# Kernel tuning notes

Measured on AMD Instinct MI355X. Metric: run time of the kernel, lower is better.

Reference implementation:

```python
import jax, jax.numpy as jnp
import numpy as np

B_SZ, L, H, D, N, R, K = 2, 1024, 2048, 4096, 16, 128, 4


def setup_inputs() -> dict:
    key = jax.random.key(0)
    ks = jax.random.split(key, 10)
    s = lambda *sh: 1.0 / np.sqrt(sh[-1])
    inp = {
        "hidden_states": jax.random.normal(ks[0], (B_SZ, L, H), jnp.float32),
        "in_proj_w": jax.random.normal(ks[1], (2 * D, H), jnp.float32) * s(H),
        "conv_w": jax.random.normal(ks[2], (D, 1, K), jnp.float32) * s(K),
        "conv_b": jax.random.normal(ks[3], (D,), jnp.float32) * 0.02,
        "x_proj_w": jax.random.normal(ks[4], (R + 2 * N, D), jnp.float32) * s(D),
        "dt_proj_w": jax.random.normal(ks[5], (D, R), jnp.float32) * s(R),
        "dt_proj_b": jax.random.normal(ks[6], (D,), jnp.float32) * 0.02,
        # A_log = log(arange(1, N+1)) broadcast over D, as in the module init
        "A_log": jnp.broadcast_to(jnp.log(jnp.arange(1, N + 1, dtype=jnp.float32))[None, :], (D, N)),
        "D_param": jnp.ones((D,), jnp.float32),
        "out_proj_w": jax.random.normal(ks[7], (H, D), jnp.float32) * s(D),
    }
    return inp


def _mamba_forward(hidden_states, in_proj_w, conv_w, conv_b, x_proj_w,
                   dt_proj_w, dt_proj_b, A_log, D_param, out_proj_w):
    silu = jax.nn.silu
    # in_proj: [B,L,H] @ [H,2D] -> [B,L,2D] -> [B,2D,L]
    proj = jnp.einsum("blh,ph->bpl", hidden_states, in_proj_w)
    u, gate = jnp.split(proj, 2, axis=1)  # each [B,D,L]
    # depthwise causal conv1d (padding K-1 on the left, then first L outputs)
    u = jax.lax.conv_general_dilated(
        u, conv_w, window_strides=(1,), padding=[(K - 1, 0)],
        dimension_numbers=("NCH", "OIH", "NCH"), feature_group_count=D,
    ) + conv_b[None, :, None]
    u = silu(u)  # [B,D,L]
    # x_proj on [B,L,D]
    ssm_params = jnp.einsum("bdl,pd->blp", u, x_proj_w)  # [B,L,R+2N]
    time_step, Bmat, Cmat = jnp.split(ssm_params, [R, R + N], axis=-1)
    # dt_proj + softplus -> [B,D,L]
    dt = jnp.einsum("blr,dr->bld", time_step, dt_proj_w) + dt_proj_b
    dt = jax.nn.softplus(dt).transpose(0, 2, 1)  # [B,D,L]
    A = -jnp.exp(A_log)  # [D,N]

    # selective scan over time; carry ssm_state [B,D,N]
    def step(state, xs):
        dt_t, B_t, C_t, u_t = xs  # [B,D],[B,N],[B,N],[B,D]
        dA = jnp.exp(A[None] * dt_t[:, :, None])          # [B,D,N]
        dBu = dt_t[:, :, None] * B_t[:, None, :] * u_t[:, :, None]
        state = dA * state + dBu
        y_t = jnp.einsum("bdn,bn->bd", state, C_t)        # [B,D]
        return state, y_t

    xs = (dt.transpose(2, 0, 1),          # [L,B,D]
          Bmat.transpose(1, 0, 2),        # [L,B,N]
          Cmat.transpose(1, 0, 2),        # [L,B,N]
          u.transpose(2, 0, 1))           # [L,B,D]
    init = jnp.zeros((hidden_states.shape[0], D, N), hidden_states.dtype)
    _, ys = jax.lax.scan(step, init, xs)   # ys [L,B,D]
    y = ys.transpose(1, 2, 0)              # [B,D,L]
    y = y + u * D_param[None, :, None]
    y = y * silu(gate)
    # out_proj: [B,L,D] @ [D,H]
    return jnp.einsum("bdl,hd->blh", y, out_proj_w)


def reference(hidden_states, in_proj_w, conv_w, conv_b, x_proj_w,
              dt_proj_w, dt_proj_b, A_log, D_param, out_proj_w):
    return _mamba_forward(hidden_states, in_proj_w, conv_w, conv_b, x_proj_w,
                          dt_proj_w, dt_proj_b, A_log, D_param, out_proj_w)
```

## Files before the change

### kernel.cpp

```cpp
#include <hip/hip_runtime.h>

#define L_SEQ 1024
#define DD 4096
#define NC 32
#define CT 32

typedef short bf16x8 __attribute__((ext_vector_type(8)));
typedef float f32x4 __attribute__((ext_vector_type(4)));
typedef unsigned short u16;

typedef const __attribute__((address_space(1))) void gas_t;
typedef __attribute__((address_space(3))) void las_t;

__device__ inline u16 f2bf(float f) {
  unsigned int u = __float_as_uint(f);
  u = (u + 0x7FFFu + ((u >> 16) & 1u)) >> 16;
  return (u16)u;
}

__device__ inline float bf2f(u16 v) {
  return __uint_as_float(((unsigned int)v) << 16);
}

__device__ inline float softplusf(float x) {
  return x > 20.f ? x : log1pf(expf(x));
}

__global__ __launch_bounds__(256) void cast_bf16_k(const float* __restrict__ s,
                                                   u16* __restrict__ d, int n) {
  int i = (blockIdx.x * 256 + threadIdx.x) * 4;
  if (i >= n) return;
  float4 v = *(const float4*)(s + i);
  ushort4 o;
  o.x = f2bf(v.x); o.y = f2bf(v.y); o.z = f2bf(v.z); o.w = f2bf(v.w);
  *(ushort4*)(d + i) = o;
}

__global__ __launch_bounds__(256) void reduce4_k(const float* __restrict__ p,
                                                 float* __restrict__ out,
                                                 long n) {
  long i = ((long)blockIdx.x * 256 + threadIdx.x) * 4;
  if (i >= n) return;
  float4 a = *(const float4*)(p + i);
  float4 b = *(const float4*)(p + n + i);
  float4 c = *(const float4*)(p + 2 * n + i);
  float4 d = *(const float4*)(p + 3 * n + i);
  float4 o;
  o.x = (a.x + b.x) + (c.x + d.x);
  o.y = (a.y + b.y) + (c.y + d.y);
  o.z = (a.z + b.z) + (c.z + d.z);
  o.w = (a.w + b.w) + (c.w + d.w);
  *(float4*)(out + i) = o;
}

template <int CMODE, bool SWZ>
__global__ __launch_bounds__(512, 2) void gemm256(const u16* __restrict__ A,
                                                  const u16* __restrict__ B,
                                                  void* __restrict__ Cv,
                                                  int Nld, int K, int kc,
                                                  long zstride) {
  __shared__ u16 lds[2][2][8192];
  const int tid = threadIdx.x;
  const int lane = tid & 63, wid = tid >> 6;
  const int wm = wid >> 2, wn = wid & 3;
  int ty = blockIdx.y, tx = blockIdx.x;
  if (SWZ) {
    int flat = blockIdx.y * 32 + blockIdx.x;
    int xcd = flat & 7, pos = flat >> 3;
    ty = (xcd & 1) * 4 + (pos >> 3);
    tx = (xcd >> 1) * 8 + (pos & 7);
  }
  const long tm = (long)ty * 256, tn = (long)tx * 256;

  const int ksw = ((lane >> 4) ^ (lane & 3) ^ ((lane >> 2) & 3)) * 8;

  const long ks0 = (CMODE == 2) ? (long)blockIdx.z * kc : 0;

  const int srow = tid >> 2;
  const u16* gA0 = A + (tm + srow) * (long)K + ks0 + ksw;
  const u16* gA1 = A + (tm + 128 + srow) * (long)K + ks0 + ksw;
  const u16* gB0 = B + (tn + srow) * (long)K + ks0 + ksw;
  const u16* gB1 = B + (tn + 128 + srow) * (long)K + ks0 + ksw;
  const int sb0 = wid * 512;
  const int sb1 = 4096 + wid * 512;

  f32x4 acc[8][4] = {};

  const int lr = lane & 15;
  const int arow = wm * 128 + lr;
  const int brow = wn * 64 + lr;

  const int KT = kc >> 5;
  int cur = 0;
  __builtin_amdgcn_global_load_lds((gas_t*)gA0, (las_t*)&lds[0][0][sb0], 16, 0, 0);
  __builtin_amdgcn_global_load_lds((gas_t*)gA1, (las_t*)&lds[0][0][sb1], 16, 0, 0);
  __builtin_amdgcn_global_load_lds((gas_t*)gB0, (las_t*)&lds[0][1][sb0], 16, 0, 0);
  __builtin_amdgcn_global_load_lds((gas_t*)gB1, (las_t*)&lds[0][1][sb1], 16, 0, 0);
  __syncthreads();

  for (int kt = 0; kt < KT; ++kt) {
    if (kt + 1 < KT) {
      const long ko = (long)(kt + 1) << 5;
      const int nb = cur ^ 1;
      __builtin_amdgcn_global_load_lds((gas_t*)(gA0 + ko), (las_t*)&lds[nb][0][sb0], 16, 0, 0);
      __builtin_amdgcn_global_load_lds((gas_t*)(gA1 + ko), (las_t*)&lds[nb][0][sb1], 16, 0, 0);
      __builtin_amdgcn_global_load_lds((gas_t*)(gB0 + ko), (las_t*)&lds[nb][1][sb0], 16, 0, 0);
      __builtin_amdgcn_global_load_lds((gas_t*)(gB1 + ko), (las_t*)&lds[nb][1][sb1], 16, 0, 0);
    }
    bf16x8 af[8], bfr[4];
#pragma unroll
    for (int n = 0; n < 4; n++)
      bfr[n] = *(const bf16x8*)&lds[cur][1][(brow + n * 16) * 32 + ksw];
#pragma unroll
    for (int m = 0; m < 8; m++)
      af[m] = *(const bf16x8*)&lds[cur][0][(arow + m * 16) * 32 + ksw];
#pragma unroll
    for (int m = 0; m < 8; m++)
#pragma unroll
      for (int n = 0; n < 4; n++)
        acc[m][n] = __builtin_amdgcn_mfma_f32_16x16x32_bf16(af[m], bfr[n],
                                                            acc[m][n], 0, 0, 0);
    __syncthreads();
    cur ^= 1;
  }

  float* Cf = (CMODE == 2) ? (float*)Cv + (long)blockIdx.z * zstride
                           : (float*)Cv;

  const int rg = (lane >> 4) * 4;
#pragma unroll
  for (int m = 0; m < 8; m++) {
    const long gr = tm + wm * 128 + m * 16 + rg;
#pragma unroll
    for (int n = 0; n < 4; n++) {
      const long gc = tn + wn * 64 + n * 16 + lr;
#pragma unroll
      for (int r = 0; r < 4; r++) {
        if (CMODE == 1)
          ((u16*)Cv)[(gr + r) * (long)Nld + gc] = f2bf(acc[m][n][r]);
        else
          Cf[(gr + r) * (long)Nld + gc] = acc[m][n][r];
      }
    }
  }
}

template <bool CLAMP_N, bool SPLITK, bool SOFTPLUS, bool OUTBF>
__global__ __launch_bounds__(256) void gemm_bt(const u16* __restrict__ A,
                                               const u16* __restrict__ B,
                                               void* __restrict__ Cv,
                                               const float* __restrict__ ebias,
                                               int Nv, int K, int ldc, int kc) {
  __shared__ u16 lA[128 * 32];
  __shared__ u16 lB[128 * 32];
  const int tid = threadIdx.x;
  const int lane = tid & 63, wid = tid >> 6;
  const int wm = wid >> 1, wn = wid & 1;
  const long tm = (long)blockIdx.y * 128, tn = (long)blockIdx.x * 128;

  f32x4 acc[4][4] = {};

  const int rowoff = lane >> 2;
  const int ko = (lane & 3) * 8;
  const int c0 = wid * 2, c1 = c0 + 1;
  const long ra0 = tm + c0 * 16 + rowoff;
  const long ra1 = tm + c1 * 16 + rowoff;
  long rb0 = tn + c0 * 16 + rowoff;
  long rb1 = tn + c1 * 16 + rowoff;
  if (CLAMP_N) {
    if (rb0 >= Nv) rb0 = Nv - 1;
    if (rb1 >= Nv) rb1 = Nv - 1;
  }
  const u16* gA0 = A + ra0 * K + ko;
  const u16* gA1 = A + ra1 * K + ko;
  const u16* gB0 = B + rb0 * K + ko;
  const u16* gB1 = B + rb1 * K + ko;
  u16* sA0 = &lA[c0 * 512];
  u16* sA1 = &lA[c1 * 512];
  u16* sB0 = &lB[c0 * 512];
  u16* sB1 = &lB[c1 * 512];

  int ks0 = 0, ks1 = K;
  if (SPLITK) { ks0 = blockIdx.z * kc; ks1 = ks0 + kc; }

  const int lr = lane & 15, kq = (lane >> 4) * 8;
  const int arow = wm * 64 + lr, brow = wn * 64 + lr;

  for (int ks = ks0; ks < ks1; ks += 32) {
    __builtin_amdgcn_global_load_lds((gas_t*)(gA0 + ks), (las_t*)sA0, 16, 0, 0);
    __builtin_amdgcn_global_load_lds((gas_t*)(gA1 + ks), (las_t*)sA1, 16, 0, 0);
    __builtin_amdgcn_global_load_lds((gas_t*)(gB0 + ks), (las_t*)sB0, 16, 0, 0);
    __builtin_amdgcn_global_load_lds((gas_t*)(gB1 + ks), (las_t*)sB1, 16, 0, 0);
    __syncthreads();
    bf16x8 af[4], bfr[4];
#pragma unroll
    for (int i = 0; i < 4; i++) {
      af[i]  = *(const bf16x8*)&lA[(arow + i * 16) * 32 + kq];
      bfr[i] = *(const bf16x8*)&lB[(brow + i * 16) * 32 + kq];
    }
#pragma unroll
    for (int i = 0; i < 4; i++)
#pragma unroll
      for (int j = 0; j < 4; j++)
        acc[i][j] = __builtin_amdgcn_mfma_f32_16x16x32_bf16(af[i], bfr[j],
                                                            acc[i][j], 0, 0, 0);
    __syncthreads();
  }

  const int rg = (lane >> 4) * 4;
#pragma unroll
  for (int i = 0; i < 4; i++) {
    const long gr = tm + wm * 64 + i * 16 + rg;
#pragma unroll
    for (int j = 0; j < 4; j++) {
      const long gc = tn + wn * 64 + j * 16 + lr;
      if (CLAMP_N && gc >= Nv) continue;
      float bias = 0.f;
      if (SOFTPLUS) bias = ebias[gc];
#pragma unroll
      for (int r = 0; r < 4; r++) {
        float v = acc[i][j][r];
        if (SOFTPLUS) v = softplusf(v + bias);
        if (SPLITK) atomicAdd((float*)Cv + (gr + r) * (long)ldc + gc, v);
        else if (OUTBF) ((u16*)Cv)[(gr + r) * (long)ldc + gc] = f2bf(v);
        else ((float*)Cv)[(gr + r) * (long)ldc + gc] = v;
      }
    }
  }
}

__global__ __launch_bounds__(256) void conv_silu_k(const u16* __restrict__ projb,
                                                   const float* __restrict__ cw,
                                                   const float* __restrict__ cb,
                                                   u16* __restrict__ ub) {
  const int idx = blockIdx.x * 256 + threadIdx.x;
  const int d = idx & (DD - 1);
  const int bl = idx >> 12;
  const int l = bl & (L_SEQ - 1);
  const float4 w = *(const float4*)(cw + d * 4);
  float s = cb[d];
  const u16* pp = projb + (long)bl * 8192 + d;
  s += w.w * bf2f(pp[0]);
  if (l >= 1) s += w.z * bf2f(pp[-8192]);
  if (l >= 2) s += w.y * bf2f(pp[-2 * 8192]);
  if (l >= 3) s += w.x * bf2f(pp[-3 * 8192]);
  const float r = s / (1.f + expf(-s));
  ub[idx] = f2bf(r);
}

__global__ __launch_bounds__(256) void ts_extract_k(const float* __restrict__ ssm,
                                                    u16* __restrict__ ts) {
  int idx = blockIdx.x * 256 + threadIdx.x;
  int row = idx >> 7, r = idx & 127;
  ts[idx] = f2bf(ssm[row * 160 + r]);
}

__global__ __launch_bounds__(256) void scan_p1(const u16* __restrict__ dt,
                                               const u16* __restrict__ u,
                                               const float* __restrict__ ssm,
                                               const float* __restrict__ A_log,
                                               float* __restrict__ Sbuf,
                                               float* __restrict__ Pbuf) {
  __shared__ float sBC[CT * 32];
  const int tid = threadIdx.x;
  const int d = blockIdx.x * 256 + tid;
  const int c = blockIdx.y, b = blockIdx.z;
  const long blbase = (long)b * L_SEQ + (long)c * CT;
  for (int i = tid; i < CT * 32; i += 256) {
    int tt = i >> 5, j = i & 31;
    sBC[i] = ssm[(blbase + tt) * 160 + 128 + j];
  }
  __syncthreads();
  float a2[16], st[16], pr[16];
#pragma unroll
  for (int g = 0; g < 4; g++) {
    float4 al = *(const float4*)(A_log + d * 16 + g * 4);
    a2[g*4+0] = -expf(al.x) * 1.4426950408889634f;
    a2[g*4+1] = -expf(al.y) * 1.4426950408889634f;
    a2[g*4+2] = -expf(al.z) * 1.4426950408889634f;
    a2[g*4+3] = -expf(al.w) * 1.4426950408889634f;
  }
#pragma unroll
  for (int n = 0; n < 16; n++) { st[n] = 0.f; pr[n] = 1.f; }
  for (int tt = 0; tt < CT; tt++) {
    const long bl = blbase + tt;
    const float dtv = bf2f(dt[bl * DD + d]);
    const float uv = bf2f(u[bl * DD + d]);
    const float dtu = dtv * uv;
    const float4* Bv = (const float4*)&sBC[tt * 32];
#pragma unroll
    for (int g = 0; g < 4; g++) {
      const float4 Bg = Bv[g];
      float e;
      e = exp2f(a2[g*4+0]*dtv); st[g*4+0] = e*st[g*4+0] + dtu*Bg.x; pr[g*4+0] *= e;
      e = exp2f(a2[g*4+1]*dtv); st[g*4+1] = e*st[g*4+1] + dtu*Bg.y; pr[g*4+1] *= e;
      e = exp2f(a2[g*4+2]*dtv); st[g*4+2] = e*st[g*4+2] + dtu*Bg.z; pr[g*4+2] *= e;
      e = exp2f(a2[g*4+3]*dtv); st[g*4+3] = e*st[g*4+3] + dtu*Bg.w; pr[g*4+3] *= e;
    }
  }
  const long base = (((long)b * NC + c) * DD + d) * 16;
#pragma unroll
  for (int g = 0; g < 4; g++) {
    *(float4*)(Sbuf + base + g * 4) = make_float4(st[g*4+0], st[g*4+1], st[g*4+2], st[g*4+3]);
    *(float4*)(Pbuf + base + g * 4) = make_float4(pr[g*4+0], pr[g*4+1], pr[g*4+2], pr[g*4+3]);
  }
}

__global__ __launch_bounds__(256) void scan_p2(const float* __restrict__ Sbuf,
                                               const float* __restrict__ Pbuf,
                                               float* __restrict__ carry) {
  const int idx = blockIdx.x * 256 + threadIdx.x;
  const int ng = idx & 3;
  const int d = (idx >> 2) & (DD - 1);
  const int b = idx >> 14;
  float4 cr = make_float4(0.f, 0.f, 0.f, 0.f);
  for (int c = 0; c < NC; c++) {
    const long base = (((long)b * NC + c) * DD + d) * 16 + ng * 4;
    *(float4*)(carry + base) = cr;
    const float4 P = *(const float4*)(Pbuf + base);
    const float4 S = *(const float4*)(Sbuf + base);
    cr.x = P.x * cr.x + S.x;
    cr.y = P.y * cr.y + S.y;
    cr.z = P.z * cr.z + S.z;
    cr.w = P.w * cr.w + S.w;
  }
}

__global__ __launch_bounds__(256) void scan_p3(const u16* __restrict__ dt,
                                               const u16* __restrict__ u,
                                               const float* __restrict__ ssm,
                                               const u16* __restrict__ projb,
                                               const float* __restrict__ A_log,
                                               const float* __restrict__ Dp,
                                               const float* __restrict__ carry,
                                               u16* __restrict__ yb) {
  __shared__ float sBC[CT * 32];
  const int tid = threadIdx.x;
  const int d = blockIdx.x * 256 + tid;
  const int c = blockIdx.y, b = blockIdx.z;
  const long blbase = (long)b * L_SEQ + (long)c * CT;
  for (int i = tid; i < CT * 32; i += 256) {
    int tt = i >> 5, j = i & 31;
    sBC[i] = ssm[(blbase + tt) * 160 + 128 + j];
  }
  __syncthreads();
  float a2[16], st[16];
#pragma unroll
  for (int g = 0; g < 4; g++) {
    float4 al = *(const float4*)(A_log + d * 16 + g * 4);
    a2[g*4+0] = -expf(al.x) * 1.4426950408889634f;
    a2[g*4+1] = -expf(al.y) * 1.4426950408889634f;
    a2[g*4+2] = -expf(al.z) * 1.4426950408889634f;
    a2[g*4+3] = -expf(al.w) * 1.4426950408889634f;
  }
  const long cbase = (((long)b * NC + c) * DD + d) * 16;
#pragma unroll
  for (int g = 0; g < 4; g++) {
    float4 cv = *(const float4*)(carry + cbase + g * 4);
    st[g*4+0] = cv.x; st[g*4+1] = cv.y; st[g*4+2] = cv.z; st[g*4+3] = cv.w;
  }
  const float dp = Dp[d];
  for (int tt = 0; tt < CT; tt++) {
    const long bl = blbase + tt;
    const float dtv = bf2f(dt[bl * DD + d]);
    const float uv = bf2f(u[bl * DD + d]);
    const float dtu = dtv * uv;
    float acc = 0.f;
    const float4* Bv = (const float4*)&sBC[tt * 32];
    const float4* Cv = Bv + 4;
#pragma unroll
    for (int g = 0; g < 4; g++) {
      const float4 Bg = Bv[g];
      const float4 Cg = Cv[g];
      float e;
      e = exp2f(a2[g*4+0]*dtv); st[g*4+0] = e*st[g*4+0] + dtu*Bg.x; acc += st[g*4+0]*Cg.x;
      e = exp2f(a2[g*4+1]*dtv); st[g*4+1] = e*st[g*4+1] + dtu*Bg.y; acc += st[g*4+1]*Cg.y;
      e = exp2f(a2[g*4+2]*dtv); st[g*4+2] = e*st[g*4+2] + dtu*Bg.z; acc += st[g*4+2]*Cg.z;
      e = exp2f(a2[g*4+3]*dtv); st[g*4+3] = e*st[g*4+3] + dtu*Bg.w; acc += st[g*4+3]*Cg.w;
    }
    const float g = bf2f(projb[bl * 8192 + DD + d]);
    const float yv = (acc + uv * dp) * (g / (1.f + expf(-g)));
    yb[bl * DD + d] = f2bf(yv);
  }
}

extern "C" void kernel_launch(void* const* d_in, const int* in_sizes, int n_in,
                              void* d_out, int out_size, void* d_ws, size_t ws_size,
                              hipStream_t stream) {
  const float* hs     = (const float*)d_in[0];
  const float* w_in   = (const float*)d_in[1];
  const float* conv_w = (const float*)d_in[2];
  const float* conv_b = (const float*)d_in[3];
  const float* xw     = (const float*)d_in[4];
  const float* dtw    = (const float*)d_in[5];
  const float* dtb    = (const float*)d_in[6];
  const float* A_log  = (const float*)d_in[7];
  const float* Dp     = (const float*)d_in[8];
  const float* ow     = (const float*)d_in[9];
  float* out = (float*)d_out;

  constexpr size_t SZ_HS_BF  = 2048ull * 2048 * 2;
  constexpr size_t SZ_WIN_BF = 8192ull * 2048 * 2;
  constexpr size_t SZ_PROJ   = 2048ull * 8192 * 2;
  constexpr size_t SZ_UBF    = 2048ull * 4096 * 2;
  constexpr size_t SZ_XW_BF  = 160ull * 4096 * 2;
  constexpr size_t SZ_SSM    = 2048ull * 160 * 4;
  constexpr size_t SZ_TS_BF  = 2048ull * 128 * 2;
  constexpr size_t SZ_DTW_BF = 4096ull * 128 * 2;
  constexpr size_t SZ_DT     = 2048ull * 4096 * 2;
  constexpr size_t SZ_OW_BF  = 2048ull * 4096 * 2;
  constexpr size_t SZ_YBF    = 2048ull * 4096 * 2;
  constexpr size_t SZ_SCAN   = 2ull * NC * DD * 16 * 4;
  constexpr size_t TOTAL = SZ_HS_BF + SZ_WIN_BF + SZ_PROJ + SZ_UBF +
                           SZ_XW_BF + SZ_SSM + SZ_TS_BF + SZ_DTW_BF + SZ_DT +
                           SZ_OW_BF + SZ_YBF + 3 * SZ_SCAN;
  if (ws_size < TOTAL) return;

  char* w = (char*)d_ws;
  u16* hs_bf   = (u16*)w;   w += SZ_HS_BF;
  u16* win_bf  = (u16*)w;   w += SZ_WIN_BF;
  u16* projb   = (u16*)w;   w += SZ_PROJ;
  u16* u_bf    = (u16*)w;   w += SZ_UBF;
  u16* xw_bf   = (u16*)w;   w += SZ_XW_BF;
  float* ssm   = (float*)w; w += SZ_SSM;
  u16* ts_bf   = (u16*)w;   w += SZ_TS_BF;
  u16* dtw_bf  = (u16*)w;   w += SZ_DTW_BF;
  u16* dt_bf   = (u16*)w;   w += SZ_DT;
  u16* ow_bf   = (u16*)w;   w += SZ_OW_BF;
  u16* y_bf    = (u16*)w;   w += SZ_YBF;
  float* Sbuf  = (float*)w; w += SZ_SCAN;
  float* Pbuf  = (float*)w; w += SZ_SCAN;
  float* carry = (float*)w; w += SZ_SCAN;

  float* parts = (float*)win_bf;

  cast_bf16_k<<<4096, 256, 0, stream>>>(hs, hs_bf, 4194304);
  cast_bf16_k<<<16384, 256, 0, stream>>>(w_in, win_bf, 16777216);
  cast_bf16_k<<<640, 256, 0, stream>>>(xw, xw_bf, 655360);
  cast_bf16_k<<<512, 256, 0, stream>>>(dtw, dtw_bf, 524288);
  cast_bf16_k<<<8192, 256, 0, stream>>>(ow, ow_bf, 8388608);

  gemm256<1, true><<<dim3(32, 8), 512, 0, stream>>>(
      hs_bf, win_bf, projb, 8192, 2048, 2048, 0);

  conv_silu_k<<<32768, 256, 0, stream>>>(projb, conv_w, conv_b, u_bf);

  hipMemsetAsync(ssm, 0, SZ_SSM, stream);
  gemm_bt<true, true, false, false><<<dim3(2, 16, 8), 256, 0, stream>>>(
      u_bf, xw_bf, ssm, nullptr, 160, 4096, 160, 512);

  ts_extract_k<<<1024, 256, 0, stream>>>(ssm, ts_bf);

  gemm_bt<false, false, true, true><<<dim3(32, 16), 256, 0, stream>>>(
      ts_bf, dtw_bf, dt_bf, dtb, 4096, 128, 4096, 0);

  scan_p1<<<dim3(16, NC, 2), 256, 0, stream>>>(dt_bf, u_bf, ssm, A_log, Sbuf, Pbuf);
  scan_p2<<<128, 256, 0, stream>>>(Sbuf, Pbuf, carry);
  scan_p3<<<dim3(16, NC, 2), 256, 0, stream>>>(dt_bf, u_bf, ssm, projb, A_log, Dp,
                                               carry, y_bf);

  gemm256<2, false><<<dim3(8, 8, 4), 512, 0, stream>>>(
      y_bf, ow_bf, parts, 2048, 4096, 1024, 2048ll * 2048);
  reduce4_k<<<4096, 256, 0, stream>>>(parts, out, 2048ll * 2048);
}
```

Baseline: 377.0 us.

## Deepen GEMM prefetch, merge cast kernels, replace atomic split-K with partial buffers

The main GEMM now keeps two K-tiles in flight. It uses explicit vmcnt waits and raw barriers, and raises wave priority around the MFMA block, so global-to-LDS loads overlap compute better. The five fp32-to-bf16 cast launches become one launch that picks its source by block index. The x_proj split-K GEMM writes per-slice partials instead of doing atomicAdd into a memset buffer. A single finalize kernel sums the slices, writes the bf16 timestep and the B/C columns, and replaces the memset and the ts_extract kernel. This trades launch overhead and atomic contention for extra workspace traffic.

```diff
diff --git a/kernel.cpp b/kernel.cpp
--- a/kernel.cpp
+++ b/kernel.cpp
@@ -26,10 +26,22 @@
   return x > 20.f ? x : log1pf(expf(x));
 }
 
-__global__ __launch_bounds__(256) void cast_bf16_k(const float* __restrict__ s,
-                                                   u16* __restrict__ d, int n) {
-  int i = (blockIdx.x * 256 + threadIdx.x) * 4;
-  if (i >= n) return;
+__global__ __launch_bounds__(256) void cast_all_k(
+    const float* __restrict__ hs, const float* __restrict__ w_in,
+    const float* __restrict__ xw, const float* __restrict__ dtw,
+    const float* __restrict__ ow, u16* __restrict__ hs_bf,
+    u16* __restrict__ win_bf, u16* __restrict__ xw_bf,
+    u16* __restrict__ dtw_bf, u16* __restrict__ ow_bf) {
+  const int blk = blockIdx.x;
+  const float* s;
+  u16* d;
+  int base;
+  if (blk < 4096)        { s = hs;   d = hs_bf;  base = blk; }
+  else if (blk < 20480)  { s = w_in; d = win_bf; base = blk - 4096; }
+  else if (blk < 21120)  { s = xw;   d = xw_bf;  base = blk - 20480; }
+  else if (blk < 21632)  { s = dtw;  d = dtw_bf; base = blk - 21120; }
+  else                   { s = ow;   d = ow_bf;  base = blk - 21632; }
+  const int i = (base * 256 + threadIdx.x) * 4;
   float4 v = *(const float4*)(s + i);
   ushort4 o;
   o.x = f2bf(v.x); o.y = f2bf(v.y); o.z = f2bf(v.z); o.w = f2bf(v.w);
@@ -51,6 +63,19 @@
   o.z = (a.z + b.z) + (c.z + d.z);
   o.w = (a.w + b.w) + (c.w + d.w);
   *(float4*)(out + i) = o;
+}
+
+__global__ __launch_bounds__(256) void xproj_fin_k(const float* __restrict__ parts,
+                                                   u16* __restrict__ ts,
+                                                   float* __restrict__ ssm) {
+  const int idx = blockIdx.x * 256 + threadIdx.x;
+  float s = 0.f;
+#pragma unroll
+  for (int z = 0; z < 8; z++) s += parts[z * 327680 + idx];
+  const int row = idx / 160;
+  const int col = idx - row * 160;
+  if (col < 128) ts[row * 128 + col] = f2bf(s);
+  else ssm[idx] = s;
 }
 
 template <int CMODE, bool SWZ>
@@ -91,38 +116,52 @@
   const int brow = wn * 64 + lr;
 
   const int KT = kc >> 5;
-  int cur = 0;
-  __builtin_amdgcn_global_load_lds((gas_t*)gA0, (las_t*)&lds[0][0][sb0], 16, 0, 0);
-  __builtin_amdgcn_global_load_lds((gas_t*)gA1, (las_t*)&lds[0][0][sb1], 16, 0, 0);
-  __builtin_amdgcn_global_load_lds((gas_t*)gB0, (las_t*)&lds[0][1][sb0], 16, 0, 0);
-  __builtin_amdgcn_global_load_lds((gas_t*)gB1, (las_t*)&lds[0][1][sb1], 16, 0, 0);
-  __syncthreads();
+
+#define STG(buf, kt)                                                           \
+  {                                                                            \
+    const long ko_ = (long)(kt) << 5;                                          \
+    __builtin_amdgcn_global_load_lds((gas_t*)(gA0 + ko_),                      \
+                                     (las_t*)&lds[buf][0][sb0], 16, 0, 0);     \
+    __builtin_amdgcn_global_load_lds((gas_t*)(gA1 + ko_),                      \
+                                     (las_t*)&lds[buf][0][sb1], 16, 0, 0);     \
+    __builtin_amdgcn_global_load_lds((gas_t*)(gB0 + ko_),                      \
+                                     (las_t*)&lds[buf][1][sb0], 16, 0, 0);     \
+    __builtin_amdgcn_global_load_lds((gas_t*)(gB1 + ko_),                      \
+                                     (las_t*)&lds[buf][1][sb1], 16, 0, 0);     \
+  }
+
+  STG(0, 0);
+  if (KT > 1) STG(1, 1);
 
   for (int kt = 0; kt < KT; ++kt) {
-    if (kt + 1 < KT) {
-      const long ko = (long)(kt + 1) << 5;
-      const int nb = cur ^ 1;
-      __builtin_amdgcn_global_load_lds((gas_t*)(gA0 + ko), (las_t*)&lds[nb][0][sb0], 16, 0, 0);
-      __builtin_amdgcn_global_load_lds((gas_t*)(gA1 + ko), (las_t*)&lds[nb][0][sb1], 16, 0, 0);
-      __builtin_amdgcn_global_load_lds((gas_t*)(gB0 + ko), (las_t*)&lds[nb][1][sb0], 16, 0, 0);
-      __builtin_amdgcn_global_load_lds((gas_t*)(gB1 + ko), (las_t*)&lds[nb][1][sb1], 16, 0, 0);
-    }
+    const int c = kt & 1;
+    if (kt + 1 < KT)
+      asm volatile("s_waitcnt vmcnt(4)" ::: "memory");
+    else
+      asm volatile("s_waitcnt vmcnt(0)" ::: "memory");
+    __builtin_amdgcn_sched_barrier(0);
+    __builtin_amdgcn_s_barrier();
     bf16x8 af[8], bfr[4];
 #pragma unroll
     for (int n = 0; n < 4; n++)
-      bfr[n] = *(const bf16x8*)&lds[cur][1][(brow + n * 16) * 32 + ksw];
+      bfr[n] = *(const bf16x8*)&lds[c][1][(brow + n * 16) * 32 + ksw];
 #pragma unroll
     for (int m = 0; m < 8; m++)
-      af[m] = *(const bf16x8*)&lds[cur][0][(arow + m * 16) * 32 + ksw];
+      af[m] = *(const bf16x8*)&lds[c][0][(arow + m * 16) * 32 + ksw];
+    __builtin_amdgcn_s_setprio(1);
 #pragma unroll
     for (int m = 0; m < 8; m++)
 #pragma unroll
       for (int n = 0; n < 4; n++)
         acc[m][n] = __builtin_amdgcn_mfma_f32_16x16x32_bf16(af[m], bfr[n],
                                                             acc[m][n], 0, 0, 0);
-    __syncthreads();
-    cur ^= 1;
-  }
+    __builtin_amdgcn_s_setprio(0);
+    __builtin_amdgcn_sched_barrier(0);
+    __builtin_amdgcn_s_barrier();
+    __builtin_amdgcn_sched_barrier(0);
+    if (kt + 2 < KT) STG(c, kt + 2);
+  }
+#undef STG
 
   float* Cf = (CMODE == 2) ? (float*)Cv + (long)blockIdx.z * zstride
                            : (float*)Cv;
@@ -145,12 +184,13 @@
   }
 }
 
-template <bool CLAMP_N, bool SPLITK, bool SOFTPLUS, bool OUTBF>
+template <bool CLAMP_N, int MODE>
 __global__ __launch_bounds__(256) void gemm_bt(const u16* __restrict__ A,
                                                const u16* __restrict__ B,
                                                void* __restrict__ Cv,
                                                const float* __restrict__ ebias,
-                                               int Nv, int K, int ldc, int kc) {
+                                               int Nv, int K, int ldc, int kc,
+                                               long zs) {
   __shared__ u16 lA[128 * 32];
   __shared__ u16 lB[128 * 32];
   const int tid = threadIdx.x;
@@ -181,7 +221,7 @@
   u16* sB1 = &lB[c1 * 512];
 
   int ks0 = 0, ks1 = K;
-  if (SPLITK) { ks0 = blockIdx.z * kc; ks1 = ks0 + kc; }
+  if (MODE == 2) { ks0 = blockIdx.z * kc; ks1 = ks0 + kc; }
 
   const int lr = lane & 15, kq = (lane >> 4) * 8;
   const int arow = wm * 64 + lr, brow = wn * 64 + lr;
@@ -207,6 +247,8 @@
     __syncthreads();
   }
 
+  float* Cf = (MODE == 2) ? (float*)Cv + (long)blockIdx.z * zs : (float*)Cv;
+
   const int rg = (lane >> 4) * 4;
 #pragma unroll
   for (int i = 0; i < 4; i++) {
@@ -216,14 +258,14 @@
       const long gc = tn + wn * 64 + j * 16 + lr;
       if (CLAMP_N && gc >= Nv) continue;
       float bias = 0.f;
-      if (SOFTPLUS) bias = ebias[gc];
+      if (MODE == 1) bias = ebias[gc];
 #pragma unroll
       for (int r = 0; r < 4; r++) {
         float v = acc[i][j][r];
-        if (SOFTPLUS) v = softplusf(v + bias);
-        if (SPLITK) atomicAdd((float*)Cv + (gr + r) * (long)ldc + gc, v);
-        else if (OUTBF) ((u16*)Cv)[(gr + r) * (long)ldc + gc] = f2bf(v);
-        else ((float*)Cv)[(gr + r) * (long)ldc + gc] = v;
+        if (MODE == 1)
+          ((u16*)Cv)[(gr + r) * (long)ldc + gc] = f2bf(softplusf(v + bias));
+        else
+          Cf[(gr + r) * (long)ldc + gc] = v;
       }
     }
   }
@@ -248,13 +290,6 @@
   ub[idx] = f2bf(r);
 }
 
-__global__ __launch_bounds__(256) void ts_extract_k(const float* __restrict__ ssm,
-                                                    u16* __restrict__ ts) {
-  int idx = blockIdx.x * 256 + threadIdx.x;
-  int row = idx >> 7, r = idx & 127;
-  ts[idx] = f2bf(ssm[row * 160 + r]);
-}
-
 __global__ __launch_bounds__(256) void scan_p1(const u16* __restrict__ dt,
                                                const u16* __restrict__ u,
                                                const float* __restrict__ ssm,
@@ -411,9 +446,10 @@
   constexpr size_t SZ_OW_BF  = 2048ull * 4096 * 2;
   constexpr size_t SZ_YBF    = 2048ull * 4096 * 2;
   constexpr size_t SZ_SCAN   = 2ull * NC * DD * 16 * 4;
+  constexpr size_t SZ_PXP    = 8ull * 2048 * 160 * 4;
   constexpr size_t TOTAL = SZ_HS_BF + SZ_WIN_BF + SZ_PROJ + SZ_UBF +
                            SZ_XW_BF + SZ_SSM + SZ_TS_BF + SZ_DTW_BF + SZ_DT +
-                           SZ_OW_BF + SZ_YBF + 3 * SZ_SCAN;
+                           SZ_OW_BF + SZ_YBF + 3 * SZ_SCAN + SZ_PXP;
   if (ws_size < TOTAL) return;
 
   char* w = (char*)d_ws;
@@ -431,28 +467,25 @@
   float* Sbuf  = (float*)w; w += SZ_SCAN;
   float* Pbuf  = (float*)w; w += SZ_SCAN;
   float* carry = (float*)w; w += SZ_SCAN;
+  float* partsx = (float*)w; w += SZ_PXP;
 
   float* parts = (float*)win_bf;
 
-  cast_bf16_k<<<4096, 256, 0, stream>>>(hs, hs_bf, 4194304);
-  cast_bf16_k<<<16384, 256, 0, stream>>>(w_in, win_bf, 16777216);
-  cast_bf16_k<<<640, 256, 0, stream>>>(xw, xw_bf, 655360);
-  cast_bf16_k<<<512, 256, 0, stream>>>(dtw, dtw_bf, 524288);
-  cast_bf16_k<<<8192, 256, 0, stream>>>(ow, ow_bf, 8388608);
+  cast_all_k<<<29824, 256, 0, stream>>>(hs, w_in, xw, dtw, ow,
+                                        hs_bf, win_bf, xw_bf, dtw_bf, ow_bf);
 
   gemm256<1, true><<<dim3(32, 8), 512, 0, stream>>>(
       hs_bf, win_bf, projb, 8192, 2048, 2048, 0);
 
   conv_silu_k<<<32768, 256, 0, stream>>>(projb, conv_w, conv_b, u_bf);
 
-  hipMemsetAsync(ssm, 0, SZ_SSM, stream);
-  gemm_bt<true, true, false, false><<<dim3(2, 16, 8), 256, 0, stream>>>(
-      u_bf, xw_bf, ssm, nullptr, 160, 4096, 160, 512);
-
-  ts_extract_k<<<1024, 256, 0, stream>>>(ssm, ts_bf);
-
-  gemm_bt<false, false, true, true><<<dim3(32, 16), 256, 0, stream>>>(
-      ts_bf, dtw_bf, dt_bf, dtb, 4096, 128, 4096, 0);
+  gemm_bt<true, 2><<<dim3(2, 16, 8), 256, 0, stream>>>(
+      u_bf, xw_bf, partsx, nullptr, 160, 4096, 160, 512, 327680);
+
+  xproj_fin_k<<<1280, 256, 0, stream>>>(partsx, ts_bf, ssm);
+
+  gemm_bt<false, 1><<<dim3(32, 16), 256, 0, stream>>>(
+      ts_bf, dtw_bf, dt_bf, dtb, 4096, 128, 4096, 0, 0);
 
   scan_p1<<<dim3(16, NC, 2), 256, 0, stream>>>(dt_bf, u_bf, ssm, A_log, Sbuf, Pbuf);
   scan_p2<<<128, 256, 0, stream>>>(Sbuf, Pbuf, carry);
```

Result: faster. 366.8 us (-2.7%).
